# Kernel optimization log

Measured on AMD Instinct MI355X. Metric: run time of the kernel, lower is better.

The kernel has to match this reference:

```python
import jax, jax.numpy as jnp
import numpy as np

SEQ_LEN = 12          # seq_length
K = 8                 # nsamples = 2 * num_samples
RADII = (4.0 + 1e-06, 8.0 + 1e-06, 12.0 + 1e-06)
COUT = (64, 128, 256)


def _group(xyz, s_xyz, radius):
    # ball query via knn + radius mask: xyz (B,N,3) queries, s_xyz (B,M,3) keys
    d2 = jnp.sum((xyz[:, :, None, :] - s_xyz[:, None, :, :]) ** 2, axis=-1)  # (B,N,M)
    neg, idx = jax.lax.top_k(-d2, K)                                          # (B,N,K)
    valid = (-neg) <= radius * radius
    # points outside the ball are replaced by the nearest neighbor (pad-with-first)
    return jnp.where(valid, idx, idx[..., :1])


def _gather(a, idx):
    # a (B,M,C), idx (B,N,K) -> (B,N,K,C)
    return jax.vmap(lambda t, i: t[i])(a, idx)


def _cell(xyz, feat, state, W, b, radius, cout):
    # PointRNN cell: group state points around current points, fuse
    # [displacement, current feature, state feature] with a shared linear,
    # then max-pool over the K neighbors. New state xyz = current xyz.
    B, N, _ = xyz.shape
    if state is None:
        s_xyz, s_feat = xyz, jnp.zeros((B, N, cout), xyz.dtype)
    else:
        s_xyz, s_feat = state
    idx = _group(xyz, s_xyz, radius)
    n_xyz = _gather(s_xyz, idx)                      # (B,N,K,3)
    n_feat = _gather(s_feat, idx)                    # (B,N,K,cout)
    disp = n_xyz - xyz[:, :, None, :]
    parts = [disp]
    if feat is not None:
        cin = feat.shape[-1]
        parts.append(jnp.broadcast_to(feat[:, :, None, :], (B, N, K, cin)))
    parts.append(n_feat)
    h = jnp.concatenate(parts, axis=-1) @ W + b      # (B,N,K,cout)
    return (xyz, jnp.max(h, axis=2))                 # (xyz, (B,N,cout))


def _forward(frames, W1, b1, W2, b2, W3, b3, Wm, bm, Wl, bl):
    half = SEQ_LEN // 2
    s1 = s2 = s3 = None
    # encode
    for i in range(half):
        s1 = _cell(frames[:, i], None, s1, W1, b1, RADII[0], COUT[0])
        s2 = _cell(s1[0], s1[1], s2, W2, b2, RADII[1], COUT[1])
        s3 = _cell(s2[0], s2[1], s3, W3, b3, RADII[2], COUT[2])
    # decode
    input_frame = frames[:, half - 1]
    preds = []
    for i in range(half, SEQ_LEN):
        s1 = _cell(input_frame, None, s1, W1, b1, RADII[0], COUT[0])
        s2 = _cell(s1[0], s1[1], s2, W2, b2, RADII[1], COUT[1])
        s3 = _cell(s2[0], s2[1], s3, W3, b3, RADII[2], COUT[2])
        h = jax.nn.relu(s3[1] @ Wm + bm)             # MLP([256,64]) = Lin+ReLU
        motion = h @ Wl + bl                         # (B,N,3)
        input_frame = input_frame + motion
        preds.append(input_frame)
    return jnp.stack(preds, axis=1)                  # (B, T/2, N, 3)


def setup_inputs() -> dict:
    key = jax.random.key(0)
    ks = jax.random.split(key, 12)
    B, N = 16, 512
    frames = jax.random.normal(ks[0], (B, SEQ_LEN, N, 3), jnp.float32) * 2.0

    def lin(k, fin, fout):
        k1, k2 = jax.random.split(k)
        s = 1.0 / np.sqrt(fin)
        return (jax.random.uniform(k1, (fin, fout), jnp.float32, -s, s),
                jax.random.uniform(k2, (fout,), jnp.float32, -s, s))

    W1, b1 = lin(ks[1], 3 + 0 + 64, 64)
    W2, b2 = lin(ks[2], 3 + 64 + 128, 128)
    W3, b3 = lin(ks[3], 3 + 128 + 256, 256)
    Wm, bm = lin(ks[4], 256, 64)
    Wl, bl = lin(ks[5], 64, 3)
    return {"frames": frames, "W1": W1, "b1": b1, "W2": W2, "b2": b2,
            "W3": W3, "b3": b3, "Wm": Wm, "bm": bm, "Wl": Wl, "bl": bl}


def reference(frames, W1, b1, W2, b2, W3, b3, Wm, bm, Wl, bl):
    return _forward(frames, W1, b1, W2, b2, W3, b3, Wm, bm, Wl, bl)
```

## Files before the change

kernel.cpp:

```cpp
#include <hip/hip_runtime.h>
#include <hip/hip_cooperative_groups.h>
#include <math.h>

namespace cg = cooperative_groups;

#define BB 16
#define NN 512
#define KNN 8
#define SEQ 12
#define TQK 16
#define QB 32
#define PB 16

typedef __attribute__((ext_vector_type(8))) short bf8_t;
typedef __attribute__((ext_vector_type(4))) float f4_t;
typedef unsigned long long ull;

__device__ __forceinline__ ushort f2b(float x) {
    uint u = __float_as_uint(x);
    return (ushort)((u + 0x7fffu + ((u >> 16) & 1u)) >> 16);
}
__device__ __forceinline__ float b2f(ushort h) {
    return __uint_as_float((uint)h << 16);
}

__device__ __forceinline__ uint ld_sys32(const ushort* p) {
    return __hip_atomic_load((const uint*)p, __ATOMIC_RELAXED,
                             __HIP_MEMORY_SCOPE_SYSTEM);
}
__device__ __forceinline__ ull ld_sys64(const void* p) {
    return __hip_atomic_load((const ull*)p, __ATOMIC_RELAXED,
                             __HIP_MEMORY_SCOPE_SYSTEM);
}
__device__ __forceinline__ int ld_sysi(const int* p) {
    return __hip_atomic_load(p, __ATOMIC_RELAXED, __HIP_MEMORY_SCOPE_SYSTEM);
}
__device__ __forceinline__ void st_sys32(ushort* p, uint v) {
    __hip_atomic_store((uint*)p, v, __ATOMIC_RELAXED,
                       __HIP_MEMORY_SCOPE_SYSTEM);
}
__device__ __forceinline__ void st_sys64(void* p, ull v) {
    __hip_atomic_store((ull*)p, v, __ATOMIC_RELAXED,
                       __HIP_MEMORY_SCOPE_SYSTEM);
}
__device__ __forceinline__ void st_sysi(int* p, int v) {
    __hip_atomic_store(p, v, __ATOMIC_RELAXED, __HIP_MEMORY_SCOPE_SYSTEM);
}
__device__ __forceinline__ void st_sysf(float* p, float v) {
    __hip_atomic_store(p, v, __ATOMIC_RELAXED, __HIP_MEMORY_SCOPE_SYSTEM);
}
__device__ __forceinline__ void st_sys_u4(ushort* p, ushort4 v) {
    union { ushort4 s; ull u; } c; c.s = v;
    st_sys64(p, c.u);
}
__device__ __forceinline__ bf8_t ld_sys_b128(const ushort* p) {
    union { ull u[2]; bf8_t v; } c;
    c.u[0] = ld_sys64(p);
    c.u[1] = ld_sys64(p + 4);
    return c.v;
}

struct CellsSM {
    float s2s[PB][132];
    float s3f[PB][260];
    float dsp[3][PB][KNN][3];
    int   jss[3][PB][KNN];
    union { ushort s1b[2][PB][72]; float hs[PB][64]; } u1;
    ushort s2b[2][PB][136];
    ushort s3c[2][PB][264];
};
union __align__(16) SM {
    CellsSM c;
    ushort  g[256 * 40 + 2 * 128 * 40];
    float   kf[1544 + 4608 + 4608];
};
union __align__(16) GKSM {
    ushort  g[256 * 40 + 2 * 128 * 40];
    float   kf[1544 + 4608 + 4608];
};

#define GRPN 64
__device__ __forceinline__ void group_barrier(int* __restrict__ bar, int g,
                                              int target, int tid) {
    __syncthreads();
    if (tid == 0) {
        __hip_atomic_fetch_add(&bar[g * 32], 1, __ATOMIC_RELAXED,
                               __HIP_MEMORY_SCOPE_SYSTEM);
        while (__hip_atomic_load(&bar[g * 32], __ATOMIC_RELAXED,
                                 __HIP_MEMORY_SCOPE_SYSTEM) < target)
            __builtin_amdgcn_s_sleep(4);
    }
    __syncthreads();
}

__device__ __forceinline__ void knn512(
        const float* __restrict__ xqp, int xq_bs,
        const float* __restrict__ xsp, int xs_bs,
        int* __restrict__ idx1, int* __restrict__ idx2, int* __restrict__ idx3,
        float r2a, float r2b, float r2c,
        int ntile, int b, float* __restrict__ smf) {
    float* s   = smf;
    float* cdp = smf + 1544;
    int*   cip = (int*)(smf + 1544 + 4608);
    const int tid = threadIdx.x;

    {
        int j = tid;
        const float* p = xsp + (long)b * xs_bs + j * 3;
        int o = 3 * j + (j >> 6);
        s[o + 0] = p[0]; s[o + 1] = p[1]; s[o + 2] = p[2];
    }
    __syncthreads();

    int qi  = tid >> 4;
    int sub = tid & 15;
    int n = ntile * QB + qi;
    const float* q = xqp + (long)b * xq_bs + n * 3;
    float qx = q[0], qy = q[1], qz2 = q[2];

    float bd[KNN];
    int   bi[KNN];
#pragma unroll
    for (int k = 0; k < KNN; ++k) { bd[k] = 1e30f; bi[k] = 0; }

    int j0 = sub * (NN / TQK);
    int sbase = 3 * j0 + (j0 >> 6);
#pragma unroll 4
    for (int jj = 0; jj < NN / TQK; ++jj) {
        float dx = s[sbase + 3 * jj + 0] - qx;
        float dy = s[sbase + 3 * jj + 1] - qy;
        float dz = s[sbase + 3 * jj + 2] - qz2;
        float d2 = fmaf(dx, dx, fmaf(dy, dy, dz * dz));
        if (d2 < bd[KNN - 1]) {
            bd[KNN - 1] = d2; bi[KNN - 1] = j0 + jj;
#pragma unroll
            for (int k = KNN - 1; k >= 1; --k) {
                if (bd[k] < bd[k - 1]) {
                    float td = bd[k]; bd[k] = bd[k - 1]; bd[k - 1] = td;
                    int   ti = bi[k]; bi[k] = bi[k - 1]; bi[k - 1] = ti;
                }
            }
        }
    }

    float* cdq = cdp + (qi * TQK + sub) * (KNN + 1);
    int*   ciq = cip + (qi * TQK + sub) * (KNN + 1);
#pragma unroll
    for (int k = 0; k < KNN; ++k) { cdq[k] = bd[k]; ciq[k] = bi[k]; }
    cdq[KNN] = 1e30f; ciq[KNN] = 0x7fffffff;
    __syncthreads();

    for (int stride = TQK / 2; stride >= 1; stride >>= 1) {
        if (sub < stride) {
            float* ca = cdp + (qi * TQK + sub) * (KNN + 1);
            float* cb = cdp + (qi * TQK + sub + stride) * (KNN + 1);
            int*   ja_p = cip + (qi * TQK + sub) * (KNN + 1);
            int*   jb_p = cip + (qi * TQK + sub + stride) * (KNN + 1);
            float rd[KNN]; int ri[KNN];
            int ia = 0, ib = 0;
#pragma unroll
            for (int k = 0; k < KNN; ++k) {
                float da = ca[ia], db = cb[ib];
                int   ja = ja_p[ia], jb = jb_p[ib];
                bool ta = (da < db) || (da == db && ja < jb);
                rd[k] = ta ? da : db; ri[k] = ta ? ja : jb;
                ia += ta ? 1 : 0; ib += ta ? 0 : 1;
            }
#pragma unroll
            for (int k = 0; k < KNN; ++k) { ca[k] = rd[k]; ja_p[k] = ri[k]; }
        }
        __syncthreads();
    }

    if (sub == 0) {
        long base = ((long)(b * NN + n)) * KNN;
        float* c0  = cdp + qi * TQK * (KNN + 1);
        int*   j0p = cip + qi * TQK * (KNN + 1);
        int i0 = j0p[0];
#pragma unroll
        for (int k = 0; k < KNN; ++k) {
            float d = c0[k]; int j = j0p[k];
            st_sysi(&idx1[base + k], (d <= r2a) ? j : i0);
            st_sysi(&idx2[base + k], (d <= r2b) ? j : i0);
            st_sysi(&idx3[base + k], (d <= r2c) ? j : i0);
        }
    }
}

template<int N, int NC>
__device__ __forceinline__ void gemmTileW(
        const ushort* __restrict__ Ah, const ushort* __restrict__ Al,
        const ushort* __restrict__ Bh, const ushort* __restrict__ Bl,
        ushort* __restrict__ G, int rb, int cb, int tid, ushort* lds) {
    const int row0 = rb * 128, c0 = cb * NC;
    ushort* ah = lds;
    ushort* al = lds + 128 * 40;
    ushort* bh = lds + 256 * 40;
    ushort* bl = lds + 256 * 40 + NC * 40;
    const int wv = tid >> 6, lane = tid & 63;
    const int m = lane & 15, quad = lane >> 4;
    const int lr = tid >> 2, ls = (tid & 3) * 8;

    f4_t acc[NC / 16];
#pragma unroll
    for (int ct = 0; ct < NC / 16; ++ct) acc[ct] = (f4_t){0.f, 0.f, 0.f, 0.f};

    bf8_t pa_h = ld_sys_b128(Ah + (long)(row0 + lr) * N + ls);
    bf8_t pa_l = ld_sys_b128(Al + (long)(row0 + lr) * N + ls);
    bf8_t pb_h, pb_l;
    const int lrB = (NC == 128) ? lr : (lr & 63);
    if (NC == 128) {
        pb_h = *(const bf8_t*)(Bh + (long)(c0 + lrB) * N + ls);
        pb_l = *(const bf8_t*)(Bl + (long)(c0 + lrB) * N + ls);
    } else {
        const ushort* Bs = (tid < 256) ? Bh : Bl;
        pb_h = *(const bf8_t*)(Bs + (long)(c0 + lrB) * N + ls);
    }

    for (int k0 = 0; k0 < N; k0 += 32) {
        __syncthreads();
        *(bf8_t*)(ah + lr * 40 + ls) = pa_h;
        *(bf8_t*)(al + lr * 40 + ls) = pa_l;
        if (NC == 128) {
            *(bf8_t*)(bh + lrB * 40 + ls) = pb_h;
            *(bf8_t*)(bl + lrB * 40 + ls) = pb_l;
        } else {
            ushort* bs = (tid < 256) ? bh : bl;
            *(bf8_t*)(bs + lrB * 40 + ls) = pb_h;
        }
        __syncthreads();
        if (k0 + 32 < N) {
            int kn = k0 + 32;
            pa_h = ld_sys_b128(Ah + (long)(row0 + lr) * N + kn + ls);
            pa_l = ld_sys_b128(Al + (long)(row0 + lr) * N + kn + ls);
            if (NC == 128) {
                pb_h = *(const bf8_t*)(Bh + (long)(c0 + lrB) * N + kn + ls);
                pb_l = *(const bf8_t*)(Bl + (long)(c0 + lrB) * N + kn + ls);
            } else {
                const ushort* Bs = (tid < 256) ? Bh : Bl;
                pb_h = *(const bf8_t*)(Bs + (long)(c0 + lrB) * N + kn + ls);
            }
        }
        bf8_t a_h = *(const bf8_t*)(ah + (wv * 16 + m) * 40 + quad * 8);
        bf8_t a_l = *(const bf8_t*)(al + (wv * 16 + m) * 40 + quad * 8);
#pragma unroll
        for (int ct = 0; ct < NC / 16; ++ct) {
            bf8_t bth = *(const bf8_t*)(bh + (ct * 16 + m) * 40 + quad * 8);
            bf8_t btl = *(const bf8_t*)(bl + (ct * 16 + m) * 40 + quad * 8);
            acc[ct] = __builtin_amdgcn_mfma_f32_16x16x32_bf16(a_h, bth, acc[ct], 0, 0, 0);
            acc[ct] = __builtin_amdgcn_mfma_f32_16x16x32_bf16(a_h, btl, acc[ct], 0, 0, 0);
            acc[ct] = __builtin_amdgcn_mfma_f32_16x16x32_bf16(a_l, bth, acc[ct], 0, 0, 0);
        }
    }
#pragma unroll
    for (int ct = 0; ct < NC / 16; ++ct) {
        int col = c0 + ct * 16 + m;
#pragma unroll
        for (int r = 0; r < 4; ++r) {
            ushort v = f2b(acc[ct][r]);
            ushort vn = (ushort)__shfl_down((int)v, 1);
            if (!(m & 1))
                st_sys32(G + (long)(row0 + wv * 16 + quad * 4 + r) * N + col,
                         (uint)v | ((uint)vn << 16));
        }
    }
}

__device__ __forceinline__ void gemm_dispatch(
        int it, int tid, ushort* lds,
        const ushort* s1h, const ushort* s1l,
        const ushort* s2h, const ushort* s2l,
        const ushort* s3h, const ushort* s3l,
        const ushort* w1h, const ushort* w1l,
        const ushort* w2h, const ushort* w2l,
        const ushort* w3h, const ushort* w3l,
        ushort* G1, ushort* G2, ushort* G3) {
    int g = it & 7, j = it >> 3;
    if (j < 16)
        gemmTileW<256, 128>(s3h, s3l, w3h, w3l, G3, g * 8 + (j & 7), j >> 3,
                            tid, lds);
    else if (j < 24)
        gemmTileW<128, 128>(s2h, s2l, w2h, w2l, G2, g * 8 + (j - 16), 0,
                            tid, lds);
    else
        gemmTileW<64, 64>(s1h, s1l, w1h, w1l, G1, g * 8 + (j - 24), 0,
                          tid, lds);
}

__device__ __forceinline__ void cells_phase(
        bool first,
        const float* __restrict__ xq, int xq_bs,
        const float* __restrict__ xs, int xs_bs,
        const int* __restrict__ i1, const int* __restrict__ i2,
        const int* __restrict__ i3,
        const ushort* __restrict__ G1p, const ushort* __restrict__ G2p,
        const ushort* __restrict__ G3p,
        ushort* __restrict__ s1h, ushort* __restrict__ s1l,
        ushort* __restrict__ s2h, ushort* __restrict__ s2l,
        ushort* __restrict__ s3h, ushort* __restrict__ s3l,
        const float* __restrict__ W1, const float* __restrict__ b1,
        const float* __restrict__ W2, const float* __restrict__ b2,
        const float* __restrict__ W3, const float* __restrict__ b3,
        const ushort* __restrict__ w2fh, const ushort* __restrict__ w2fl,
        const ushort* __restrict__ w3fh, const ushort* __restrict__ w3fl,
        const ushort* __restrict__ wmh, const ushort* __restrict__ wml,
        const float* __restrict__ bm,
        const float* __restrict__ Wl, const float* __restrict__ bl,
        float* __restrict__ xnext, int xn_bs, int do_head,
        int blk, int tid, CellsSM& sm) {
    const int xcd = blk & 7, slot = blk >> 3;
    const int b   = xcd * 2 + (slot >> 5);
    const int n0  = (slot & 31) << 4;
    const long row0 = (long)b * NN + n0;
    const long bN = (long)b * NN;
    const int wv = tid >> 6, lane = tid & 63;
    const int fm = lane & 15, quad = lane >> 4;

    for (int t = tid; t < 3 * PB * KNN; t += 512) {
        int r = t >> 7, rem = t & 127, p = rem >> 3, k = rem & 7;
        const int* ix = (r == 0) ? i1 : ((r == 1) ? i2 : i3);
        int j = ld_sysi(&ix[(row0 + p) * KNN + k]);
        sm.jss[r][p][k] = j;
        const float* sp = xs + (long)b * xs_bs + j * 3;
        const float* qp = xq + (long)b * xq_bs + (n0 + p) * 3;
        sm.dsp[r][p][k][0] = sp[0] - qp[0];
        sm.dsp[r][p][k][1] = sp[1] - qp[1];
        sm.dsp[r][p][k][2] = sp[2] - qp[2];
    }
    __syncthreads();

    {
        int co = tid & 63, q = tid >> 6;
        float g1r[2][KNN];
        if (!first) {
#pragma unroll
            for (int r = 0; r < 2; ++r)
#pragma unroll
                for (int k = 0; k < KNN; ++k) {
                    uint vv = ld_sys32(G1p + (bN + sm.jss[0][2 * q + r][k]) * 64
                                       + (co & ~1));
                    ushort hv = (co & 1) ? (ushort)(vv >> 16) : (ushort)vv;
                    g1r[r][k] = b2f(hv);
                }
        }
        float wx = W1[co], wy = W1[64 + co], wz = W1[128 + co];
        float bz = b1[co];
#pragma unroll
        for (int r = 0; r < 2; ++r) {
            int p = 2 * q + r;
            float acc = -1e30f;
#pragma unroll
            for (int k = 0; k < KNN; ++k) {
                float v = fmaf(sm.dsp[0][p][k][0], wx, bz);
                v = fmaf(sm.dsp[0][p][k][1], wy, v);
                v = fmaf(sm.dsp[0][p][k][2], wz, v);
                if (!first) v += g1r[r][k];
                acc = fmaxf(acc, v);
            }
            ushort h = f2b(acc);
            ushort l = f2b(acc - b2f(h));
            sm.u1.s1b[0][p][co] = h;
            sm.u1.s1b[1][p][co] = l;
            ushort hn = (ushort)__shfl_down((int)h, 1);
            ushort ln = (ushort)__shfl_down((int)l, 1);
            if (!(co & 1)) {
                st_sys32(s1h + (row0 + p) * 64 + co, (uint)h | ((uint)hn << 16));
                st_sys32(s1l + (row0 + p) * 64 + co, (uint)l | ((uint)ln << 16));
            }
        }
    }
    __syncthreads();

    float4 g2r[KNN];
    {
        int c4 = tid & 31, g = tid >> 5;
        if (!first) {
#pragma unroll
            for (int k = 0; k < KNN; ++k) {
                ull v = ld_sys64(&G2p[(bN + sm.jss[1][g][k]) * 128 + c4 * 4]);
                g2r[k] = make_float4(b2f((ushort)v), b2f((ushort)(v >> 16)),
                                     b2f((ushort)(v >> 32)), b2f((ushort)(v >> 48)));
            }
        }
    }

    {
        int col = wv * 16 + fm;
        float bz = b2[col];
        f4_t acc = {bz, bz, bz, bz};
#pragma unroll
        for (int k0 = 0; k0 < 64; k0 += 32) {
            bf8_t ah = *(const bf8_t*)&sm.u1.s1b[0][fm][k0 + quad * 8];
            bf8_t al = *(const bf8_t*)&sm.u1.s1b[1][fm][k0 + quad * 8];
            bf8_t bh = *(const bf8_t*)(w2fh + col * 64 + k0 + quad * 8);
            bf8_t bl = *(const bf8_t*)(w2fl + col * 64 + k0 + quad * 8);
            acc = __builtin_amdgcn_mfma_f32_16x16x32_bf16(ah, bh, acc, 0, 0, 0);
            acc = __builtin_amdgcn_mfma_f32_16x16x32_bf16(ah, bl, acc, 0, 0, 0);
            acc = __builtin_amdgcn_mfma_f32_16x16x32_bf16(al, bh, acc, 0, 0, 0);
        }
#pragma unroll
        for (int r = 0; r < 4; ++r) sm.s2s[quad * 4 + r][col] = acc[r];
    }
    __syncthreads();

    {
        int c4 = tid & 31, g = tid >> 5;
        float4 bse = *(float4*)&sm.s2s[g][c4 * 4];
        float4 wx = ((const float4*)W2)[c4];
        float4 wy = ((const float4*)(W2 + 128))[c4];
        float4 wz = ((const float4*)(W2 + 256))[c4];
        float4 m = make_float4(-1e30f, -1e30f, -1e30f, -1e30f);
#pragma unroll
        for (int k = 0; k < KNN; ++k) {
            float dx = sm.dsp[1][g][k][0], dy = sm.dsp[1][g][k][1],
                  dz = sm.dsp[1][g][k][2];
            float4 v;
            v.x = fmaf(dz, wz.x, fmaf(dy, wy.x, fmaf(dx, wx.x, bse.x)));
            v.y = fmaf(dz, wz.y, fmaf(dy, wy.y, fmaf(dx, wx.y, bse.y)));
            v.z = fmaf(dz, wz.z, fmaf(dy, wy.z, fmaf(dx, wx.z, bse.z)));
            v.w = fmaf(dz, wz.w, fmaf(dy, wy.w, fmaf(dx, wx.w, bse.w)));
            if (!first) {
                v.x += g2r[k].x; v.y += g2r[k].y;
                v.z += g2r[k].z; v.w += g2r[k].w;
            }
            m.x = fmaxf(m.x, v.x); m.y = fmaxf(m.y, v.y);
            m.z = fmaxf(m.z, v.z); m.w = fmaxf(m.w, v.w);
        }
        ushort4 mh, ml;
        mh.x = f2b(m.x); ml.x = f2b(m.x - b2f(mh.x));
        mh.y = f2b(m.y); ml.y = f2b(m.y - b2f(mh.y));
        mh.z = f2b(m.z); ml.z = f2b(m.z - b2f(mh.z));
        mh.w = f2b(m.w); ml.w = f2b(m.w - b2f(mh.w));
        *(ushort4*)&sm.s2b[0][g][c4 * 4] = mh;
        *(ushort4*)&sm.s2b[1][g][c4 * 4] = ml;
        st_sys_u4(&s2h[(row0 + g) * 128 + c4 * 4], mh);
        st_sys_u4(&s2l[(row0 + g) * 128 + c4 * 4], ml);
    }
    __syncthreads();

    float4 g3r[2][KNN];
    {
        int c4 = tid & 63, g = tid >> 6;
        if (!first) {
#pragma unroll
            for (int r = 0; r < 2; ++r)
#pragma unroll
                for (int k = 0; k < KNN; ++k) {
                    ull v = ld_sys64(&G3p[(bN + sm.jss[2][2 * g + r][k]) * 256 + c4 * 4]);
                    g3r[r][k] = make_float4(b2f((ushort)v), b2f((ushort)(v >> 16)),
                                            b2f((ushort)(v >> 32)), b2f((ushort)(v >> 48)));
                }
        }
    }

    {
        int col0 = wv * 16 + fm, col1 = (wv + 8) * 16 + fm;
        float bz0 = b3[col0], bz1 = b3[col1];
        f4_t a0 = {bz0, bz0, bz0, bz0};
        f4_t a1 = {bz1, bz1, bz1, bz1};
#pragma unroll
        for (int k0 = 0; k0 < 128; k0 += 32) {
            bf8_t ah = *(const bf8_t*)&sm.s2b[0][fm][k0 + quad * 8];
            bf8_t al = *(const bf8_t*)&sm.s2b[1][fm][k0 + quad * 8];
            bf8_t b0h = *(const bf8_t*)(w3fh + col0 * 128 + k0 + quad * 8);
            bf8_t b0l = *(const bf8_t*)(w3fl + col0 * 128 + k0 + quad * 8);
            bf8_t b1h = *(const bf8_t*)(w3fh + col1 * 128 + k0 + quad * 8);
            bf8_t b1l = *(const bf8_t*)(w3fl + col1 * 128 + k0 + quad * 8);
            a0 = __builtin_amdgcn_mfma_f32_16x16x32_bf16(ah, b0h, a0, 0, 0, 0);
            a0 = __builtin_amdgcn_mfma_f32_16x16x32_bf16(ah, b0l, a0, 0, 0, 0);
            a0 = __builtin_amdgcn_mfma_f32_16x16x32_bf16(al, b0h, a0, 0, 0, 0);
            a1 = __builtin_amdgcn_mfma_f32_16x16x32_bf16(ah, b1h, a1, 0, 0, 0);
            a1 = __builtin_amdgcn_mfma_f32_16x16x32_bf16(ah, b1l, a1, 0, 0, 0);
            a1 = __builtin_amdgcn_mfma_f32_16x16x32_bf16(al, b1h, a1, 0, 0, 0);
        }
#pragma unroll
        for (int r = 0; r < 4; ++r) {
            sm.s3f[quad * 4 + r][col0] = a0[r];
            sm.s3f[quad * 4 + r][col1] = a1[r];
        }
    }
    __syncthreads();

    {
        int c4 = tid & 63, g = tid >> 6;
        float4 wx = ((const float4*)W3)[c4];
        float4 wy = ((const float4*)(W3 + 256))[c4];
        float4 wz = ((const float4*)(W3 + 512))[c4];
#pragma unroll
        for (int r = 0; r < 2; ++r) {
            int p = 2 * g + r;
            float4 bse = *(float4*)&sm.s3f[p][c4 * 4];
            float4 m = make_float4(-1e30f, -1e30f, -1e30f, -1e30f);
#pragma unroll
            for (int k = 0; k < KNN; ++k) {
                float dx = sm.dsp[2][p][k][0], dy = sm.dsp[2][p][k][1],
                      dz = sm.dsp[2][p][k][2];
                float4 v;
                v.x = fmaf(dz, wz.x, fmaf(dy, wy.x, fmaf(dx, wx.x, bse.x)));
                v.y = fmaf(dz, wz.y, fmaf(dy, wy.y, fmaf(dx, wx.y, bse.y)));
                v.z = fmaf(dz, wz.z, fmaf(dy, wy.z, fmaf(dx, wx.z, bse.z)));
                v.w = fmaf(dz, wz.w, fmaf(dy, wy.w, fmaf(dx, wx.w, bse.w)));
                if (!first) {
                    v.x += g3r[r][k].x; v.y += g3r[r][k].y;
                    v.z += g3r[r][k].z; v.w += g3r[r][k].w;
                }
                m.x = fmaxf(m.x, v.x); m.y = fmaxf(m.y, v.y);
                m.z = fmaxf(m.z, v.z); m.w = fmaxf(m.w, v.w);
            }
            ushort4 mh, ml;
            mh.x = f2b(m.x); ml.x = f2b(m.x - b2f(mh.x));
            mh.y = f2b(m.y); ml.y = f2b(m.y - b2f(mh.y));
            mh.z = f2b(m.z); ml.z = f2b(m.z - b2f(mh.z));
            mh.w = f2b(m.w); ml.w = f2b(m.w - b2f(mh.w));
            *(ushort4*)&sm.s3c[0][p][c4 * 4] = mh;
            *(ushort4*)&sm.s3c[1][p][c4 * 4] = ml;
            st_sys_u4(&s3h[(row0 + p) * 256 + c4 * 4], mh);
            st_sys_u4(&s3l[(row0 + p) * 256 + c4 * 4], ml);
        }
    }

    if (do_head) {
        __syncthreads();
        if (wv < 4) {
            int col = wv * 16 + fm;
            float bz = bm[col];
            f4_t acc = {bz, bz, bz, bz};
#pragma unroll
            for (int k0 = 0; k0 < 256; k0 += 32) {
                bf8_t ah = *(const bf8_t*)&sm.s3c[0][fm][k0 + quad * 8];
                bf8_t al = *(const bf8_t*)&sm.s3c[1][fm][k0 + quad * 8];
                bf8_t bh = *(const bf8_t*)(wmh + col * 256 + k0 + quad * 8);
                bf8_t bl = *(const bf8_t*)(wml + col * 256 + k0 + quad * 8);
                acc = __builtin_amdgcn_mfma_f32_16x16x32_bf16(ah, bh, acc, 0, 0, 0);
                acc = __builtin_amdgcn_mfma_f32_16x16x32_bf16(ah, bl, acc, 0, 0, 0);
                acc = __builtin_amdgcn_mfma_f32_16x16x32_bf16(al, bh, acc, 0, 0, 0);
            }
            __syncthreads();
#pragma unroll
            for (int r = 0; r < 4; ++r)
                sm.u1.hs[quad * 4 + r][col] = fmaxf(acc[r], 0.f);
        } else {
            __syncthreads();
        }
        __syncthreads();
        if (tid < PB * 3) {
            int p = tid / 3, d = tid % 3;
            float m = bl[d];
#pragma unroll 4
            for (int c = 0; c < 64; ++c)
                m = fmaf(sm.u1.hs[p][c], Wl[c * 3 + d], m);
            const float* qp = xq + (long)b * xq_bs + (n0 + p) * 3;
            st_sysf(&xnext[(long)b * xn_bs + (n0 + p) * 3 + d], qp[d] + m);
        }
    }
}

__device__ __forceinline__ void convW_one(int id,
        const float* __restrict__ W1, const float* __restrict__ W2,
        const float* __restrict__ W3, const float* __restrict__ Wm,
        ushort* w1h, ushort* w1l, ushort* w2h, ushort* w2l,
        ushort* w3h, ushort* w3l, ushort* w2fh, ushort* w2fl,
        ushort* w3fh, ushort* w3fl, ushort* wmh, ushort* wml) {
    float v; ushort* ph; ushort* pl; int idx;
    if (id < 4096)        { int n = id >> 6, k = id & 63;
        v = W1[(3 + k) * 64 + n];   ph = w1h;  pl = w1l;  idx = id; }
    else if (id < 20480)  { int u = id - 4096, n = u >> 7, k = u & 127;
        v = W2[(67 + k) * 128 + n]; ph = w2h;  pl = w2l;  idx = u; }
    else if (id < 86016)  { int u = id - 20480, n = u >> 8, k = u & 255;
        v = W3[(131 + k) * 256 + n]; ph = w3h; pl = w3l;  idx = u; }
    else if (id < 94208)  { int u = id - 86016, n = u >> 6, k = u & 63;
        v = W2[(3 + k) * 128 + n];  ph = w2fh; pl = w2fl; idx = u; }
    else if (id < 126976) { int u = id - 94208, n = u >> 7, k = u & 127;
        v = W3[(3 + k) * 256 + n];  ph = w3fh; pl = w3fl; idx = u; }
    else if (id < 143360) { int u = id - 126976, n = u >> 8, k = u & 255;
        v = Wm[k * 64 + n];         ph = wmh;  pl = wml;  idx = u; }
    else return;
    ushort h = f2b(v);
    ph[idx] = h; pl[idx] = f2b(v - b2f(h));
}

__global__ __launch_bounds__(512, 4) void fused_kernel(
        const float* frames, float* out,
        ushort* G1, ushort* G2, ushort* G3,
        ushort* s1h, ushort* s1l, ushort* s2h, ushort* s2l,
        ushort* s3h, ushort* s3l,
        ushort* w1h, ushort* w1l, ushort* w2h, ushort* w2l,
        ushort* w3h, ushort* w3l,
        ushort* w2fh, ushort* w2fl, ushort* w3fh, ushort* w3fl,
        ushort* wmh, ushort* wml,
        int* idx1w, int* idx2w, int* idx3w, int* bar,
        const float* W1, const float* b1, const float* W2, const float* b2,
        const float* W3, const float* b3, const float* Wm, const float* bm,
        const float* Wl, const float* bl,
        float r2a, float r2b, float r2c) {
    __shared__ SM sm;
    cg::grid_group grid = cg::this_grid();
    const int bx = blockIdx.x, tid = threadIdx.x;
    const int grp = bx & 7;
    const int FB = SEQ * NN * 3, OB = 6 * NN * 3;
    const long BNK = (long)BB * NN * KNN;

    if (bx == 0 && tid < 8) st_sysi(&bar[tid * 32], 0);
    convW_one(bx * 512 + tid, W1, W2, W3, Wm,
              w1h, w1l, w2h, w2l, w3h, w3l,
              w2fh, w2fl, w3fh, w3fl, wmh, wml);
    if (bx < 256) {
        int xcd = bx & 7, slot = bx >> 3;
        int b = xcd * 2 + (slot & 1), ntile = slot >> 1;
        knn512(frames, FB, frames, FB, idx1w, idx2w, idx3w,
               r2a, r2b, r2c, ntile, b, sm.kf);
    }
    grid.sync();

    int ph = 1;

    for (int t = 0; t < SEQ; ++t) {
        const float* xq; int xq_bs; const float* xs; int xs_bs;
        if (t < 6)       { xq = frames + (long)t * NN * 3;        xq_bs = FB; }
        else if (t == 6) { xq = frames + 5L * NN * 3;             xq_bs = FB; }
        else             { xq = out + (long)(t - 7) * NN * 3;     xq_bs = OB; }
        if (t == 0)      { xs = xq;                               xs_bs = xq_bs; }
        else if (t <= 6) { xs = frames + (long)(t - 1) * NN * 3;  xs_bs = FB; }
        else if (t == 7) { xs = frames + 5L * NN * 3;             xs_bs = FB; }
        else             { xs = out + (long)(t - 8) * NN * 3;     xs_bs = OB; }
        int slot = (t <= 6) ? t : 0;
        const int* i1 = idx1w + slot * BNK;
        const int* i2 = idx2w + slot * BNK;
        const int* i3 = idx3w + slot * BNK;
        int do_head = (t >= 6);
        float* xnext = do_head ? out + (long)(t - 6) * NN * 3 : nullptr;

        cells_phase(t == 0, xq, xq_bs, xs, xs_bs, i1, i2, i3,
                    G1, G2, G3, s1h, s1l, s2h, s2l, s3h, s3l,
                    W1, b1, W2, b2, W3, b3,
                    w2fh, w2fl, w3fh, w3fl, wmh, wml, bm,
                    Wl, bl, xnext, OB, do_head, bx, tid, sm.c);

        if (t == SEQ - 1) break;
        group_barrier(bar, grp, GRPN * ph, tid); ++ph;

        if (bx < 256) {
            int tn = t + 1;
            const float* kq; int kq_bs; const float* ksp; int ks_bs; int kslot;
            if (tn <= 6) {
                int qz = tn < 5 ? tn : 5;
                kq = frames + (long)qz * NN * 3;        kq_bs = FB;
                ksp = frames + (long)(tn - 1) * NN * 3; ks_bs = FB;
                kslot = tn;
            } else {
                kq = out + (long)(tn - 7) * NN * 3;     kq_bs = OB;
                if (tn == 7) { ksp = frames + 5L * NN * 3;          ks_bs = FB; }
                else         { ksp = out + (long)(tn - 8) * NN * 3; ks_bs = OB; }
                kslot = 0;
            }
            int xcd = bx & 7, slot2 = bx >> 3;
            int b = xcd * 2 + (slot2 & 1), ntile = slot2 >> 1;
            knn512(kq, kq_bs, ksp, ks_bs,
                   idx1w + (long)kslot * BNK, idx2w + (long)kslot * BNK,
                   idx3w + (long)kslot * BNK,
                   r2a, r2b, r2c, ntile, b, sm.kf);
        } else {
            gemm_dispatch(bx - 256, tid, sm.g,
                          s1h, s1l, s2h, s2l, s3h, s3l,
                          w1h, w1l, w2h, w2l, w3h, w3l, G1, G2, G3);
        }
        group_barrier(bar, grp, GRPN * ph, tid); ++ph;
    }
}

__global__ __launch_bounds__(512) void init512_kernel(
        const float* __restrict__ frames, int FB,
        int* __restrict__ i1, int* __restrict__ i2, int* __restrict__ i3,
        float r2a, float r2b, float r2c,
        const float* __restrict__ W1, const float* __restrict__ W2,
        const float* __restrict__ W3, const float* __restrict__ Wm,
        ushort* w1h, ushort* w1l, ushort* w2h, ushort* w2l,
        ushort* w3h, ushort* w3l, ushort* w2fh, ushort* w2fl,
        ushort* w3fh, ushort* w3fl, ushort* wmh, ushort* wml) {
    __shared__ float kf[1544 + 4608 + 4608];
    int bx = blockIdx.x;
    if (bx < 256) {
        int xcd = bx & 7, slot = bx >> 3;
        int b = xcd * 2 + (slot & 1), ntile = slot >> 1;
        knn512(frames, FB, frames, FB, i1, i2, i3, r2a, r2b, r2c,
               ntile, b, kf);
        return;
    }
    convW_one((bx - 256) * 512 + threadIdx.x, W1, W2, W3, Wm,
              w1h, w1l, w2h, w2l, w3h, w3l,
              w2fh, w2fl, w3fh, w3fl, wmh, wml);
}

__global__ __launch_bounds__(512) void cells512_kernel(
        int first,
        const float* __restrict__ xq, int xq_bs,
        const float* __restrict__ xs, int xs_bs,
        const int* __restrict__ i1, const int* __restrict__ i2,
        const int* __restrict__ i3,
        const ushort* __restrict__ G1p, const ushort* __restrict__ G2p,
        const ushort* __restrict__ G3p,
        ushort* s1h, ushort* s1l, ushort* s2h, ushort* s2l,
        ushort* s3h, ushort* s3l,
        const float* __restrict__ W1, const float* __restrict__ b1,
        const float* __restrict__ W2, const float* __restrict__ b2,
        const float* __restrict__ W3, const float* __restrict__ b3,
        const ushort* __restrict__ w2fh, const ushort* __restrict__ w2fl,
        const ushort* __restrict__ w3fh, const ushort* __restrict__ w3fl,
        const ushort* __restrict__ wmh, const ushort* __restrict__ wml,
        const float* __restrict__ bm,
        const float* __restrict__ Wl, const float* __restrict__ bl,
        float* xnext, int xn_bs, int do_head) {
    __shared__ CellsSM sm;
    cells_phase(first != 0, xq, xq_bs, xs, xs_bs, i1, i2, i3,
                G1p, G2p, G3p, s1h, s1l, s2h, s2l, s3h, s3l,
                W1, b1, W2, b2, W3, b3, w2fh, w2fl, w3fh, w3fl,
                wmh, wml, bm, Wl, bl, xnext, xn_bs, do_head,
                blockIdx.x, threadIdx.x, sm);
}

__global__ __launch_bounds__(512) void gemmknn512_kernel(
        const ushort* s1h, const ushort* s1l,
        const ushort* s2h, const ushort* s2l,
        const ushort* s3h, const ushort* s3l,
        const ushort* w1h, const ushort* w1l,
        const ushort* w2h, const ushort* w2l,
        const ushort* w3h, const ushort* w3l,
        ushort* G1, ushort* G2, ushort* G3,
        const float* __restrict__ kq, int kq_bs,
        const float* __restrict__ ks, int ks_bs,
        int* ki1, int* ki2, int* ki3,
        float r2a, float r2b, float r2c) {
    __shared__ GKSM sm;
    int bx = blockIdx.x, tid = threadIdx.x;
    if (bx < 256) {
        int xcd = bx & 7, slot = bx >> 3;
        int b = xcd * 2 + (slot & 1), ntile = slot >> 1;
        knn512(kq, kq_bs, ks, ks_bs, ki1, ki2, ki3, r2a, r2b, r2c,
               ntile, b, sm.kf);
        return;
    }
    gemm_dispatch(bx - 256, tid, sm.g,
                  s1h, s1l, s2h, s2l, s3h, s3l,
                  w1h, w1l, w2h, w2l, w3h, w3l, G1, G2, G3);
}

extern "C" void kernel_launch(void* const* d_in, const int* in_sizes, int n_in,
                              void* d_out, int out_size, void* d_ws, size_t ws_size,
                              hipStream_t stream) {
    const float* frames = (const float*)d_in[0];
    const float* W1 = (const float*)d_in[1]; const float* b1 = (const float*)d_in[2];
    const float* W2 = (const float*)d_in[3]; const float* b2 = (const float*)d_in[4];
    const float* W3 = (const float*)d_in[5]; const float* b3 = (const float*)d_in[6];
    const float* Wm = (const float*)d_in[7]; const float* bm = (const float*)d_in[8];
    const float* Wl = (const float*)d_in[9]; const float* bl = (const float*)d_in[10];
    float* out = (float*)d_out;

    const long M = (long)BB * NN;
    ushort* us = (ushort*)d_ws;
    ushort* G1b = us; us += M * 64;
    ushort* G2b = us; us += M * 128;
    ushort* G3b = us; us += M * 256;
    ushort* s1h = us; us += M * 64;   ushort* s1l = us; us += M * 64;
    ushort* s2h = us; us += M * 128;  ushort* s2l = us; us += M * 128;
    ushort* s3h = us; us += M * 256;  ushort* s3l = us; us += M * 256;
    ushort* w1h = us; us += 4096;     ushort* w1l = us; us += 4096;
    ushort* w2h = us; us += 16384;    ushort* w2l = us; us += 16384;
    ushort* w3h = us; us += 65536;    ushort* w3l = us; us += 65536;
    ushort* w2fh = us; us += 8192;    ushort* w2fl = us; us += 8192;
    ushort* w3fh = us; us += 32768;   ushort* w3fl = us; us += 32768;
    ushort* wmh = us; us += 16384;    ushort* wml = us; us += 16384;
    us += (size_t)us & 1;
    const long BNK = M * KNN;
    int* ip = (int*)us;
    int* idx1w = ip; ip += 7 * BNK;
    int* idx2w = ip; ip += 7 * BNK;
    int* idx3w = ip; ip += 7 * BNK;
    int* bar   = ip; ip += 8 * 32;

    double ra = 4.0 + 1e-6, rbd = 8.0 + 1e-6, rc = 12.0 + 1e-6;
    float r2a = (float)(ra * ra), r2b = (float)(rbd * rbd), r2c = (float)(rc * rc);

    const int FB = SEQ * NN * 3;
    const int OB = 6 * NN * 3;

    static int g_coop = -1;
    if (g_coop < 0) {
        int attr = 0, dev = 0, nb = 0;
        hipGetDevice(&dev);
        hipDeviceGetAttribute(&attr, hipDeviceAttributeCooperativeLaunch, dev);
        hipDeviceProp_t prop{};
        hipGetDeviceProperties(&prop, dev);
        if (attr &&
            hipOccupancyMaxActiveBlocksPerMultiprocessor(
                &nb, fused_kernel, 512, 0) == hipSuccess &&
            nb * prop.multiProcessorCount >= 512)
            g_coop = 1;
        else
            g_coop = 0;
    }

    bool did_coop = false;
    if (g_coop == 1) {
        void* args[] = {
            (void*)&frames, (void*)&out,
            (void*)&G1b, (void*)&G2b, (void*)&G3b,
            (void*)&s1h, (void*)&s1l, (void*)&s2h, (void*)&s2l,
            (void*)&s3h, (void*)&s3l,
            (void*)&w1h, (void*)&w1l, (void*)&w2h, (void*)&w2l,
            (void*)&w3h, (void*)&w3l,
            (void*)&w2fh, (void*)&w2fl, (void*)&w3fh, (void*)&w3fl,
            (void*)&wmh, (void*)&wml,
            (void*)&idx1w, (void*)&idx2w, (void*)&idx3w, (void*)&bar,
            (void*)&W1, (void*)&b1, (void*)&W2, (void*)&b2,
            (void*)&W3, (void*)&b3, (void*)&Wm, (void*)&bm,
            (void*)&Wl, (void*)&bl,
            (void*)&r2a, (void*)&r2b, (void*)&r2c
        };
        hipError_t e = hipLaunchCooperativeKernel((const void*)fused_kernel,
                                                  dim3(512), dim3(512),
                                                  args, 0, stream);
        did_coop = (e == hipSuccess);
        if (!did_coop) g_coop = 0;
    }

    if (!did_coop) {
        init512_kernel<<<536, 512, 0, stream>>>(
            frames, FB, idx1w, idx2w, idx3w, r2a, r2b, r2c,
            W1, W2, W3, Wm, w1h, w1l, w2h, w2l, w3h, w3l,
            w2fh, w2fl, w3fh, w3fl, wmh, wml);

        for (int t = 0; t < SEQ; ++t) {
            const float* xq; int xq_bs; const float* xs; int xs_bs;
            if (t < 6)       { xq = frames + (long)t * NN * 3;        xq_bs = FB; }
            else if (t == 6) { xq = frames + 5L * NN * 3;             xq_bs = FB; }
            else             { xq = out + (long)(t - 7) * NN * 3;     xq_bs = OB; }
            if (t == 0)      { xs = xq;                               xs_bs = xq_bs; }
            else if (t <= 6) { xs = frames + (long)(t - 1) * NN * 3;  xs_bs = FB; }
            else if (t == 7) { xs = frames + 5L * NN * 3;             xs_bs = FB; }
            else             { xs = out + (long)(t - 8) * NN * 3;     xs_bs = OB; }

            int slot = (t <= 6) ? t : 0;
            int* i1 = idx1w + (long)slot * BNK;
            int* i2 = idx2w + (long)slot * BNK;
            int* i3 = idx3w + (long)slot * BNK;

            int do_head = (t >= 6);
            float* xnext = do_head ? out + (long)(t - 6) * NN * 3 : nullptr;

            cells512_kernel<<<BB * NN / PB, 512, 0, stream>>>(
                t == 0 ? 1 : 0, xq, xq_bs, xs, xs_bs, i1, i2, i3,
                G1b, G2b, G3b, s1h, s1l, s2h, s2l, s3h, s3l,
                W1, b1, W2, b2, W3, b3,
                w2fh, w2fl, w3fh, w3fl, wmh, wml, bm,
                Wl, bl, xnext, OB, do_head);

            if (t < SEQ - 1) {
                int tn = t + 1;
                const float* kq; int kq_bs; const float* ksp; int ks_bs; int kslot;
                if (tn <= 6) {
                    int qz = tn < 5 ? tn : 5;
                    kq = frames + (long)qz * NN * 3;        kq_bs = FB;
                    ksp = frames + (long)(tn - 1) * NN * 3; ks_bs = FB;
                    kslot = tn;
                } else {
                    kq = out + (long)(tn - 7) * NN * 3;     kq_bs = OB;
                    if (tn == 7) { ksp = frames + 5L * NN * 3;          ks_bs = FB; }
                    else         { ksp = out + (long)(tn - 8) * NN * 3; ks_bs = OB; }
                    kslot = 0;
                }
                gemmknn512_kernel<<<512, 512, 0, stream>>>(
                    s1h, s1l, s2h, s2l, s3h, s3l,
                    w1h, w1l, w2h, w2l, w3h, w3l,
                    G1b, G2b, G3b,
                    kq, kq_bs, ksp, ks_bs,
                    idx1w + (long)kslot * BNK, idx2w + (long)kslot * BNK,
                    idx3w + (long)kslot * BNK,
                    r2a, r2b, r2c);
            }
        }
    }
}
```

Before: 510.9 us.

## Precompute encode-phase KNN one step ahead and prefill neighbor displacements

The persistent kernel now runs the KNN for frame 1 alongside frame 0 in the prologue, using the otherwise-idle upper blocks. During the encode steps it computes the KNN for step t+2, since query frames are known ahead of time. The per-step displacement and index fill (p0) moves out of the cells phase into the tail of the preceding barrier phase, kept in a separate persistent shared-memory struct. This shortens the critical path of each cells phase, at the cost of more shared memory per block and extra per-step idx buffer slots.

```diff
diff --git a/kernel.cpp b/kernel.cpp
--- a/kernel.cpp
+++ b/kernel.cpp
@@ -60,21 +60,19 @@
     return c.v;
 }
 
-struct CellsSM {
+struct PersistSM {
+    float dsp[3][PB][KNN][3];
+    int   jss[3][PB][KNN];
+};
+struct CellsRest {
     float s2s[PB][132];
     float s3f[PB][260];
-    float dsp[3][PB][KNN][3];
-    int   jss[3][PB][KNN];
     union { ushort s1b[2][PB][72]; float hs[PB][64]; } u1;
     ushort s2b[2][PB][136];
     ushort s3c[2][PB][264];
 };
-union __align__(16) SM {
-    CellsSM c;
-    ushort  g[256 * 40 + 2 * 128 * 40];
-    float   kf[1544 + 4608 + 4608];
-};
-union __align__(16) GKSM {
+union __align__(16) SMU {
+    CellsRest c;
     ushort  g[256 * 40 + 2 * 128 * 40];
     float   kf[1544 + 4608 + 4608];
 };
@@ -184,6 +182,25 @@
             st_sysi(&idx2[base + k], (d <= r2b) ? j : i0);
             st_sysi(&idx3[base + k], (d <= r2c) ? j : i0);
         }
+    }
+}
+
+__device__ __forceinline__ void p0_fill(
+        const float* __restrict__ xq, int xq_bs,
+        const float* __restrict__ xs, int xs_bs,
+        const int* __restrict__ i1, const int* __restrict__ i2,
+        const int* __restrict__ i3,
+        int b, int n0, long row0, int tid, PersistSM& ps) {
+    for (int t = tid; t < 3 * PB * KNN; t += 512) {
+        int r = t >> 7, rem = t & 127, p = rem >> 3, k = rem & 7;
+        const int* ix = (r == 0) ? i1 : ((r == 1) ? i2 : i3);
+        int j = ld_sysi(&ix[(row0 + p) * KNN + k]);
+        ps.jss[r][p][k] = j;
+        const float* sp = xs + (long)b * xs_bs + j * 3;
+        const float* qp = xq + (long)b * xq_bs + (n0 + p) * 3;
+        ps.dsp[r][p][k][0] = sp[0] - qp[0];
+        ps.dsp[r][p][k][1] = sp[1] - qp[1];
+        ps.dsp[r][p][k][2] = sp[2] - qp[2];
     }
 }
 
@@ -288,7 +305,7 @@
 }
 
 __device__ __forceinline__ void cells_phase(
-        bool first,
+        bool first, int skip_p0,
         const float* __restrict__ xq, int xq_bs,
         const float* __restrict__ xs, int xs_bs,
         const int* __restrict__ i1, const int* __restrict__ i2,
@@ -307,7 +324,7 @@
         const float* __restrict__ bm,
         const float* __restrict__ Wl, const float* __restrict__ bl,
         float* __restrict__ xnext, int xn_bs, int do_head,
-        int blk, int tid, CellsSM& sm) {
+        int blk, int tid, PersistSM& ps, CellsRest& sm) {
     const int xcd = blk & 7, slot = blk >> 3;
     const int b   = xcd * 2 + (slot >> 5);
     const int n0  = (slot & 31) << 4;
@@ -316,18 +333,10 @@
     const int wv = tid >> 6, lane = tid & 63;
     const int fm = lane & 15, quad = lane >> 4;
 
-    for (int t = tid; t < 3 * PB * KNN; t += 512) {
-        int r = t >> 7, rem = t & 127, p = rem >> 3, k = rem & 7;
-        const int* ix = (r == 0) ? i1 : ((r == 1) ? i2 : i3);
-        int j = ld_sysi(&ix[(row0 + p) * KNN + k]);
-        sm.jss[r][p][k] = j;
-        const float* sp = xs + (long)b * xs_bs + j * 3;
-        const float* qp = xq + (long)b * xq_bs + (n0 + p) * 3;
-        sm.dsp[r][p][k][0] = sp[0] - qp[0];
-        sm.dsp[r][p][k][1] = sp[1] - qp[1];
-        sm.dsp[r][p][k][2] = sp[2] - qp[2];
-    }
-    __syncthreads();
+    if (!skip_p0) {
+        p0_fill(xq, xq_bs, xs, xs_bs, i1, i2, i3, b, n0, row0, tid, ps);
+        __syncthreads();
+    }
 
     {
         int co = tid & 63, q = tid >> 6;
@@ -337,7 +346,7 @@
             for (int r = 0; r < 2; ++r)
 #pragma unroll
                 for (int k = 0; k < KNN; ++k) {
-                    uint vv = ld_sys32(G1p + (bN + sm.jss[0][2 * q + r][k]) * 64
+                    uint vv = ld_sys32(G1p + (bN + ps.jss[0][2 * q + r][k]) * 64
                                        + (co & ~1));
                     ushort hv = (co & 1) ? (ushort)(vv >> 16) : (ushort)vv;
                     g1r[r][k] = b2f(hv);
@@ -351,9 +360,9 @@
             float acc = -1e30f;
 #pragma unroll
             for (int k = 0; k < KNN; ++k) {
-                float v = fmaf(sm.dsp[0][p][k][0], wx, bz);
-                v = fmaf(sm.dsp[0][p][k][1], wy, v);
-                v = fmaf(sm.dsp[0][p][k][2], wz, v);
+                float v = fmaf(ps.dsp[0][p][k][0], wx, bz);
+                v = fmaf(ps.dsp[0][p][k][1], wy, v);
+                v = fmaf(ps.dsp[0][p][k][2], wz, v);
                 if (!first) v += g1r[r][k];
                 acc = fmaxf(acc, v);
             }
@@ -377,7 +386,7 @@
         if (!first) {
 #pragma unroll
             for (int k = 0; k < KNN; ++k) {
-                ull v = ld_sys64(&G2p[(bN + sm.jss[1][g][k]) * 128 + c4 * 4]);
+                ull v = ld_sys64(&G2p[(bN + ps.jss[1][g][k]) * 128 + c4 * 4]);
                 g2r[k] = make_float4(b2f((ushort)v), b2f((ushort)(v >> 16)),
                                      b2f((ushort)(v >> 32)), b2f((ushort)(v >> 48)));
             }
@@ -412,8 +421,8 @@
         float4 m = make_float4(-1e30f, -1e30f, -1e30f, -1e30f);
 #pragma unroll
         for (int k = 0; k < KNN; ++k) {
-            float dx = sm.dsp[1][g][k][0], dy = sm.dsp[1][g][k][1],
-                  dz = sm.dsp[1][g][k][2];
+            float dx = ps.dsp[1][g][k][0], dy = ps.dsp[1][g][k][1],
+                  dz = ps.dsp[1][g][k][2];
             float4 v;
             v.x = fmaf(dz, wz.x, fmaf(dy, wy.x, fmaf(dx, wx.x, bse.x)));
             v.y = fmaf(dz, wz.y, fmaf(dy, wy.y, fmaf(dx, wx.y, bse.y)));
@@ -446,7 +455,7 @@
             for (int r = 0; r < 2; ++r)
 #pragma unroll
                 for (int k = 0; k < KNN; ++k) {
-                    ull v = ld_sys64(&G3p[(bN + sm.jss[2][2 * g + r][k]) * 256 + c4 * 4]);
+                    ull v = ld_sys64(&G3p[(bN + ps.jss[2][2 * g + r][k]) * 256 + c4 * 4]);
                     g3r[r][k] = make_float4(b2f((ushort)v), b2f((ushort)(v >> 16)),
                                             b2f((ushort)(v >> 32)), b2f((ushort)(v >> 48)));
                 }
@@ -493,8 +502,8 @@
             float4 m = make_float4(-1e30f, -1e30f, -1e30f, -1e30f);
 #pragma unroll
             for (int k = 0; k < KNN; ++k) {
-                float dx = sm.dsp[2][p][k][0], dy = sm.dsp[2][p][k][1],
-                      dz = sm.dsp[2][p][k][2];
+                float dx = ps.dsp[2][p][k][0], dy = ps.dsp[2][p][k][1],
+                      dz = ps.dsp[2][p][k][2];
                 float4 v;
                 v.x = fmaf(dz, wz.x, fmaf(dy, wy.x, fmaf(dx, wx.x, bse.x)));
                 v.y = fmaf(dz, wz.y, fmaf(dy, wy.y, fmaf(dx, wx.y, bse.y)));
@@ -593,22 +602,34 @@
         const float* W3, const float* b3, const float* Wm, const float* bm,
         const float* Wl, const float* bl,
         float r2a, float r2b, float r2c) {
-    __shared__ SM sm;
+    __shared__ PersistSM ps;
+    __shared__ SMU smu;
     cg::grid_group grid = cg::this_grid();
     const int bx = blockIdx.x, tid = threadIdx.x;
     const int grp = bx & 7;
     const int FB = SEQ * NN * 3, OB = 6 * NN * 3;
     const long BNK = (long)BB * NN * KNN;
 
+    const int c_xcd = bx & 7, c_slot = bx >> 3;
+    const int c_b = c_xcd * 2 + (c_slot >> 5);
+    const int c_n0 = (c_slot & 31) << 4;
+    const long c_row0 = (long)c_b * NN + c_n0;
+
     if (bx == 0 && tid < 8) st_sysi(&bar[tid * 32], 0);
     convW_one(bx * 512 + tid, W1, W2, W3, Wm,
               w1h, w1l, w2h, w2l, w3h, w3l,
               w2fh, w2fl, w3fh, w3fl, wmh, wml);
-    if (bx < 256) {
-        int xcd = bx & 7, slot = bx >> 3;
+    {
+        int r = bx & 255;
+        int xcd = r & 7, slot = r >> 3;
         int b = xcd * 2 + (slot & 1), ntile = slot >> 1;
-        knn512(frames, FB, frames, FB, idx1w, idx2w, idx3w,
-               r2a, r2b, r2c, ntile, b, sm.kf);
+        if (bx < 256)
+            knn512(frames, FB, frames, FB, idx1w, idx2w, idx3w,
+                   r2a, r2b, r2c, ntile, b, smu.kf);
+        else
+            knn512(frames + (long)NN * 3, FB, frames, FB,
+                   idx1w + BNK, idx2w + BNK, idx3w + BNK,
+                   r2a, r2b, r2c, ntile, b, smu.kf);
     }
     grid.sync();
 
@@ -628,41 +649,58 @@
         const int* i2 = idx2w + slot * BNK;
         const int* i3 = idx3w + slot * BNK;
         int do_head = (t >= 6);
+        int skip_p0 = (t >= 1 && t <= 6);
         float* xnext = do_head ? out + (long)(t - 6) * NN * 3 : nullptr;
 
-        cells_phase(t == 0, xq, xq_bs, xs, xs_bs, i1, i2, i3,
+        cells_phase(t == 0, skip_p0, xq, xq_bs, xs, xs_bs, i1, i2, i3,
                     G1, G2, G3, s1h, s1l, s2h, s2l, s3h, s3l,
                     W1, b1, W2, b2, W3, b3,
                     w2fh, w2fl, w3fh, w3fl, wmh, wml, bm,
-                    Wl, bl, xnext, OB, do_head, bx, tid, sm.c);
+                    Wl, bl, xnext, OB, do_head, bx, tid, ps, smu.c);
 
         if (t == SEQ - 1) break;
         group_barrier(bar, grp, GRPN * ph, tid); ++ph;
 
         if (bx < 256) {
-            int tn = t + 1;
-            const float* kq; int kq_bs; const float* ksp; int ks_bs; int kslot;
-            if (tn <= 6) {
-                int qz = tn < 5 ? tn : 5;
-                kq = frames + (long)qz * NN * 3;        kq_bs = FB;
-                ksp = frames + (long)(tn - 1) * NN * 3; ks_bs = FB;
-                kslot = tn;
-            } else {
-                kq = out + (long)(tn - 7) * NN * 3;     kq_bs = OB;
+            if (t <= 4) {
+                int z = t + 2;
+                int qz = z < 5 ? z : 5;
+                int xcd = bx & 7, slot2 = bx >> 3;
+                int b = xcd * 2 + (slot2 & 1), ntile = slot2 >> 1;
+                knn512(frames + (long)qz * NN * 3, FB,
+                       frames + (long)(z - 1) * NN * 3, FB,
+                       idx1w + (long)z * BNK, idx2w + (long)z * BNK,
+                       idx3w + (long)z * BNK,
+                       r2a, r2b, r2c, ntile, b, smu.kf);
+            } else if (t >= 6) {
+                int tn = t + 1;
+                const float* kq = out + (long)(tn - 7) * NN * 3;
+                const float* ksp; int ks_bs;
                 if (tn == 7) { ksp = frames + 5L * NN * 3;          ks_bs = FB; }
                 else         { ksp = out + (long)(tn - 8) * NN * 3; ks_bs = OB; }
-                kslot = 0;
-            }
-            int xcd = bx & 7, slot2 = bx >> 3;
-            int b = xcd * 2 + (slot2 & 1), ntile = slot2 >> 1;
-            knn512(kq, kq_bs, ksp, ks_bs,
-                   idx1w + (long)kslot * BNK, idx2w + (long)kslot * BNK,
-                   idx3w + (long)kslot * BNK,
-                   r2a, r2b, r2c, ntile, b, sm.kf);
+                int xcd = bx & 7, slot2 = bx >> 3;
+                int b = xcd * 2 + (slot2 & 1), ntile = slot2 >> 1;
+                knn512(kq, OB, ksp, ks_bs, idx1w, idx2w, idx3w,
+                       r2a, r2b, r2c, ntile, b, smu.kf);
+            }
         } else {
-            gemm_dispatch(bx - 256, tid, sm.g,
+            gemm_dispatch(bx - 256, tid, smu.g,
                           s1h, s1l, s2h, s2l, s3h, s3l,
                           w1h, w1l, w2h, w2l, w3h, w3l, G1, G2, G3);
+        }
+
+        {
+            int tn = t + 1;
+            if (tn <= 6) {
+                const float* pq = (tn < 6) ? frames + (long)tn * NN * 3
+                                           : frames + 5L * NN * 3;
+                const float* psrc = frames + (long)(tn - 1) * NN * 3;
+                __syncthreads();
+                p0_fill(pq, FB, psrc, FB,
+                        idx1w + (long)tn * BNK, idx2w + (long)tn * BNK,
+                        idx3w + (long)tn * BNK,
+                        c_b, c_n0, c_row0, tid, ps);
+            }
         }
         group_barrier(bar, grp, GRPN * ph, tid); ++ph;
     }
@@ -710,12 +748,13 @@
         const float* __restrict__ bm,
         const float* __restrict__ Wl, const float* __restrict__ bl,
         float* xnext, int xn_bs, int do_head) {
-    __shared__ CellsSM sm;
-    cells_phase(first != 0, xq, xq_bs, xs, xs_bs, i1, i2, i3,
+    __shared__ PersistSM ps;
+    __shared__ CellsRest sm;
+    cells_phase(first != 0, 0, xq, xq_bs, xs, xs_bs, i1, i2, i3,
                 G1p, G2p, G3p, s1h, s1l, s2h, s2l, s3h, s3l,
                 W1, b1, W2, b2, W3, b3, w2fh, w2fl, w3fh, w3fl,
                 wmh, wml, bm, Wl, bl, xnext, xn_bs, do_head,
-                blockIdx.x, threadIdx.x, sm);
+                blockIdx.x, threadIdx.x, ps, sm);
 }
 
 __global__ __launch_bounds__(512) void gemmknn512_kernel(
@@ -730,16 +769,16 @@
         const float* __restrict__ ks, int ks_bs,
         int* ki1, int* ki2, int* ki3,
         float r2a, float r2b, float r2c) {
-    __shared__ GKSM sm;
+    __shared__ SMU smu;
     int bx = blockIdx.x, tid = threadIdx.x;
     if (bx < 256) {
         int xcd = bx & 7, slot = bx >> 3;
         int b = xcd * 2 + (slot & 1), ntile = slot >> 1;
         knn512(kq, kq_bs, ks, ks_bs, ki1, ki2, ki3, r2a, r2b, r2c,
-               ntile, b, sm.kf);
+               ntile, b, smu.kf);
         return;
     }
-    gemm_dispatch(bx - 256, tid, sm.g,
+    gemm_dispatch(bx - 256, tid, smu.g,
                   s1h, s1l, s2h, s2l, s3h, s3l,
                   w1h, w1l, w2h, w2l, w3h, w3l, G1, G2, G3);
 }
```

Result: slower. 548.8 us (+7.4%).
